# Performance work log

Measured on AMD Instinct MI355X. Metric: run time of the kernel, lower is better.

## Reference

```python
import jax, jax.numpy as jnp
import numpy as np

B, T, D_IN = 32, 32, 128
N_SLOTS, M_LEN = 512, 64
NUM_SHIFT, NUM_READ, NUM_WRITE = 3, 4, 1
CTRL_DIM = 256
READ_HEAD_LEN = 3 + M_LEN + NUM_SHIFT            # k, beta, g, s, gamma
WRITE_HEAD_LEN = READ_HEAD_LEN + 2 * M_LEN       # + erase, add vectors
INSTR_DIM = NUM_READ * READ_HEAD_LEN + NUM_WRITE * WRITE_HEAD_LEN


def setup_inputs() -> dict:
    key = jax.random.key(0)
    ks = jax.random.split(key, 4)
    def glorot(k, shape):
        lim = np.sqrt(6.0 / (shape[0] + shape[1])).astype(np.float32)
        return jax.random.uniform(k, shape, jnp.float32, -lim, lim)
    return {
        "x": jax.random.normal(ks[0], (B, T, D_IN), jnp.float32),
        "Wc": glorot(ks[1], (D_IN + NUM_READ * M_LEN, CTRL_DIM)),
        "bc": jnp.zeros((CTRL_DIM,), jnp.float32),
        "heads_kernel": glorot(ks[2], (CTRL_DIM, INSTR_DIM)),
        "heads_bias": jnp.zeros((INSTR_DIM,), jnp.float32),
    }


def _parse_heads(h):
    # h: (B, H, 3 + M + S) -> k, beta, g, s, gamma per _get_weight_vector
    k = h[..., :M_LEN]
    b = jnp.exp(h[..., M_LEN])
    g = jax.nn.sigmoid(h[..., M_LEN + 1])
    s = jax.nn.softmax(h[..., M_LEN + 2:M_LEN + 2 + NUM_SHIFT], axis=-1)
    t = jax.nn.softplus(h[..., M_LEN + 2 + NUM_SHIFT]) + 1.0
    return k, b, g, s, t


def _address(Mem, w_prev, k, b, g, s, t):
    # Mem:(B,N,M) k:(B,H,M) w_prev:(B,H,N) b,g,t:(B,H) s:(B,H,S)
    eps = 1e-8
    Mn = jnp.linalg.norm(Mem, axis=-1)                       # (B,N)
    kn = jnp.linalg.norm(k, axis=-1)                         # (B,H)
    sim = jnp.einsum('bhm,bnm->bhn', k, Mem) / (kn[..., None] * Mn[:, None, :] + eps)
    wc = jax.nn.softmax(b[..., None] * sim, axis=-1)         # content
    wg = g[..., None] * wc + (1.0 - g[..., None]) * w_prev   # gate
    half = NUM_SHIFT // 2                                    # circular shift conv
    wsh = sum(s[..., i:i + 1] * jnp.roll(wg, i - half, axis=-1) for i in range(NUM_SHIFT))
    wt = wsh ** t[..., None]                                 # sharpen
    return wt / (jnp.sum(wt, axis=-1, keepdims=True) + eps)


def _ntm_forward(x, Wc, bc, heads_kernel, heads_bias):
    def step(carry, x_t):
        r, rw, ww, Mem = carry
        # dense controller on [x_t, old read vectors]
        ctrl_in = jnp.concatenate([x_t, r.reshape(B, -1)], axis=-1)
        h = jnp.tanh(ctrl_in @ Wc + bc)                      # controller_out == instr
        instr = h @ heads_kernel + heads_bias                # (B, INSTR_DIM)
        rh = instr[:, :NUM_READ * READ_HEAD_LEN].reshape(B, NUM_READ, READ_HEAD_LEN)
        wh = instr[:, NUM_READ * READ_HEAD_LEN:].reshape(B, NUM_WRITE, WRITE_HEAD_LEN)
        rw_n = _address(Mem, rw, *_parse_heads(rh))
        ww_n = _address(Mem, ww, *_parse_heads(wh[..., :READ_HEAD_LEN]))
        e = wh[..., READ_HEAD_LEN:READ_HEAD_LEN + M_LEN]     # raw erase (no sigmoid, as in source)
        a = wh[..., READ_HEAD_LEN + M_LEN:]                  # raw add
        # erase all heads, then add all heads (source loops erase first)
        Mem = Mem * jnp.prod(1.0 - ww_n[..., :, None] * e[..., None, :], axis=1)
        Mem = Mem + jnp.einsum('bwn,bwm->bnm', ww_n, a)
        r_n = jnp.einsum('bnm,brn->brm', Mem, rw_n)          # read
        return (r_n, rw_n, ww_n, Mem), h

    init = (jnp.zeros((B, NUM_READ, M_LEN), jnp.float32),
            jnp.zeros((B, NUM_READ, N_SLOTS), jnp.float32),
            jnp.zeros((B, NUM_WRITE, N_SLOTS), jnp.float32),
            jnp.zeros((B, N_SLOTS, M_LEN), jnp.float32))
    _, outs = jax.lax.scan(step, init, jnp.swapaxes(x, 0, 1))  # time-major
    return outs[-1]  # return_sequences=False -> last controller output (B, CTRL_DIM)


def reference(x, Wc, bc, heads_kernel, heads_bias):
    return _ntm_forward(x, Wc, bc, heads_kernel, heads_bias)
```

## Files before the change

### kernel.cpp

```cpp
#include <hip/hip_runtime.h>
#include <math.h>

#define BB 32
#define TT 32
#define D_INX 128
#define NSLOT 512
#define MLEN 64
#define NREAD 4
#define NHEAD 5
#define CDIM 256
#define IDIM 478
#define NT 1024

#define HKB_OFF 196608


struct SMem {
    float mem[NSLOT * MLEN];
    float wread4[NSLOT * 4];
    float wwrite[NSLOT];
    float mn[NSLOT];
    float ctrl[512];
    float h[CDIM];
    float instr[480];
    float xpart[CDIM];
    float u[2560];
};

__device__ __forceinline__ unsigned short f2bf(float f) {
    unsigned u = __float_as_uint(f);
    return (unsigned short)((u + 0x7fffu + ((u >> 16) & 1u)) >> 16);
}

__device__ __forceinline__ int permcol(int c) {
    if (c < 280) { int h = c / 70, m = c - h * 70;
        return (m < 64) ? h * 64 + m : 448 + h * 6 + (m - 64); }
    if (c < 344) return 256 + (c - 280);
    if (c < 350) return 472 + (c - 344);
    if (c < 414) return 320 + (c - 350);
    return 384 + (c - 414);
}

__global__ void pack_kernel(const float* __restrict__ Wc, const float* __restrict__ Hk,
                            unsigned short* __restrict__ wctb, unsigned short* __restrict__ hkb)
{
    int idx = blockIdx.x * 256 + threadIdx.x;
    if (idx < 384 * 256) {
        int i = idx >> 8, col = idx & 255;
        wctb[((i >> 3) * 256 + col) * 8 + (i & 7)] = f2bf(Wc[idx]);
    }
    if (idx < 256 * 478) {
        int i = idx / 478, c = idx - i * 478;
        hkb[((i >> 3) * 478 + permcol(c)) * 8 + (i & 7)] = f2bf(Hk[idx]);
    }
}

#define BFU_DOT(wv, cA, cB, acc) do {                                           \
    unsigned _u0 = (wv).x, _u1 = (wv).y, _u2 = (wv).z, _u3 = (wv).w;            \
    acc += __uint_as_float(_u0 << 16) * (cA).x + __uint_as_float(_u0 & 0xffff0000u) * (cA).y; \
    acc += __uint_as_float(_u1 << 16) * (cA).z + __uint_as_float(_u1 & 0xffff0000u) * (cA).w; \
    acc += __uint_as_float(_u2 << 16) * (cB).x + __uint_as_float(_u2 & 0xffff0000u) * (cB).y; \
    acc += __uint_as_float(_u3 << 16) * (cB).z + __uint_as_float(_u3 & 0xffff0000u) * (cB).w; \
} while (0)

#define L2E 1.4426950408889634f
#define LN2 0.6931471805599453f

__global__ __launch_bounds__(NT, 4)
void ntm_kernel(const float* __restrict__ x,
                const float* __restrict__ bc,
                const float* __restrict__ hb,
                const unsigned short* __restrict__ wctb,
                const unsigned short* __restrict__ hkb,
                float* __restrict__ out)
{
    extern __shared__ float smem_f[];
    SMem* sc = (SMem*)smem_f;

    const int b    = blockIdx.x;
    const int tid  = threadIdx.x;
    const int lane = tid & 63;
    const int wave = tid >> 6;

    float hbv = 0.f;
    if (tid >= 256 && tid < 256 + IDIM) {
        int j = tid - 256, c;
        if (j < 320) { int h = j >> 6, m = j & 63; c = (h < 4) ? h * 70 + m : 280 + m; }
        else if (j < 384) c = 350 + (j - 320);
        else if (j < 448) c = 414 + (j - 384);
        else { int q = j - 448; int h = q / 6, i = q - h * 6;
               c = (h < 4) ? h * 70 + 64 + i : 344 + i; }
        hbv = hb[c];
    }
    float bcv1 = (tid < CDIM) ? bc[tid] : 0.f;
    float bcv4 = (tid >= 320 && tid < 576) ? bc[tid - 320] : 0.f;

    {
        float4 z4 = make_float4(0.f, 0.f, 0.f, 0.f);
        float4* m4 = (float4*)sc->mem;
        for (int i = tid; i < NSLOT * MLEN / 4; i += NT) m4[i] = z4;
        if (tid < NSLOT) {
            ((float4*)sc->wread4)[tid] = z4;
            sc->wwrite[tid] = 0.f;
            sc->mn[tid] = 0.f;
            sc->ctrl[tid] = (tid < D_INX) ? x[(size_t)b * TT * D_INX + tid] : 0.f;
        }
    }
    __syncthreads();
    if (tid < CDIM) {
        const uint4* wq = (const uint4*)wctb + tid;
        const float4* xa = (const float4*)sc->ctrl;
        float acc = bcv1;
#pragma unroll
        for (int cc = 0; cc < 16; ++cc) {
            uint4 wv = wq[cc * 256];
            BFU_DOT(wv, xa[2 * cc], xa[2 * cc + 1], acc);
        }
        sc->xpart[tid] = acc;
    }
    __syncthreads();

    for (int t = 0; t < TT; ++t) {
        {
            int col = tid & 255, kb = tid >> 8;
            const uint4* wq = (const uint4*)wctb + (16 + kb * 8) * 256 + col;
            const float4* ra = (const float4*)(sc->ctrl + 256) + kb * 16;
            float acc = 0.f;
#pragma unroll
            for (int cc = 0; cc < 8; ++cc) {
                uint4 wv = wq[cc * 256];
                BFU_DOT(wv, ra[2 * cc], ra[2 * cc + 1], acc);
            }
            sc->u[kb * 256 + col] = acc;
        }
        __syncthreads();

        if (tid < CDIM) {
            float acc = sc->xpart[tid] + sc->u[tid] + sc->u[256 + tid]
                      + sc->u[512 + tid] + sc->u[768 + tid];
            float av = fabsf(acc);
            float ex = __builtin_amdgcn_exp2f(av * (2.f * L2E));
            float r1 = 1.f - 2.f / (ex + 1.f);
            float hv = (acc < 0.f) ? -r1 : r1;
            sc->h[tid] = hv;
            if (t == TT - 1) out[(size_t)b * CDIM + tid] = hv;
        } else if (tid < 256 + IDIM) {
            sc->instr[tid - 256] = hbv;
        }
        if (t == TT - 1) break;
        __syncthreads();

        {
            int col = tid & 511, kb = tid >> 9;
            if (col < IDIM) {
                const uint4* wq = (const uint4*)hkb + kb * 16 * IDIM + col;
                const float4* h4 = (const float4*)sc->h + kb * 32;
                float acc = 0.f;
#pragma unroll
                for (int cc = 0; cc < 16; ++cc) {
                    uint4 wv = wq[cc * IDIM];
                    BFU_DOT(wv, h4[2 * cc], h4[2 * cc + 1], acc);
                }
                atomicAdd(&sc->instr[col], acc);
            } else if (tid >= 990 && tid < 1022) {
                int i = tid - 990;
                ((float4*)(sc->ctrl + (((t + 1) & 1) << 7)))[i] =
                    ((const float4*)(x + ((size_t)b * TT + t + 1) * D_INX))[i];
            }
        }
        __syncthreads();

        {
            int n = tid >> 1, half = tid & 1, nx = n & 15;
            const float4* m4 = (const float4*)sc->mem + n * 16;
            const float4* kb4 = (const float4*)sc->instr;
            float d0 = 0.f, d1 = 0.f, d2 = 0.f, d3 = 0.f, d4 = 0.f;
#pragma unroll
            for (int jj = 0; jj < 8; ++jj) {
                int j = half * 8 + jj;
                float4 mv = m4[j ^ nx];
                float4 k0 = kb4[j], k1 = kb4[16 + j], k2 = kb4[32 + j],
                       k3 = kb4[48 + j], kw = kb4[64 + j];
                d0 += mv.x * k0.x + mv.y * k0.y + mv.z * k0.z + mv.w * k0.w;
                d1 += mv.x * k1.x + mv.y * k1.y + mv.z * k1.z + mv.w * k1.w;
                d2 += mv.x * k2.x + mv.y * k2.y + mv.z * k2.z + mv.w * k2.w;
                d3 += mv.x * k3.x + mv.y * k3.y + mv.z * k3.z + mv.w * k3.w;
                d4 += mv.x * kw.x + mv.y * kw.y + mv.z * kw.z + mv.w * kw.w;
            }
            d0 += __shfl_xor(d0, 1); d1 += __shfl_xor(d1, 1); d2 += __shfl_xor(d2, 1);
            d3 += __shfl_xor(d3, 1); d4 += __shfl_xor(d4, 1);
            if (half == 0) {
                sc->u[n] = d0; sc->u[512 + n] = d1; sc->u[1024 + n] = d2;
                sc->u[1536 + n] = d3; sc->u[2048 + n] = d4;
            }
        }
        __syncthreads();

        if (wave < NHEAD) {
            const int h = wave;
            const float* sb = sc->instr + 448 + h * 6;
            float kv = sc->instr[h * 64 + lane];
            float sq = kv * kv;
#pragma unroll
            for (int off = 32; off; off >>= 1) sq += __shfl_xor(sq, off);
            float kn = sqrtf(sq);
            float beta = __expf(sb[0]);
            float g = 1.f / (1.f + __expf(-sb[1]));
            float v0 = sb[2], v1 = sb[3], v2 = sb[4];
            float mx3 = fmaxf(v0, fmaxf(v1, v2));
            float e0 = __expf(v0 - mx3), e1 = __expf(v1 - mx3), e2 = __expf(v2 - mx3);
            float inv3 = 1.f / (e0 + e1 + e2);
            float s0 = e0 * inv3, s1 = e1 * inv3, s2 = e2 * inv3;
            float tv = sb[5];
            float tp = fmaxf(tv, 0.f)
                     + LN2 * __builtin_amdgcn_logf(1.f + __builtin_amdgcn_exp2f(-fabsf(tv) * L2E))
                     + 1.f;

            float uu[8];
#pragma unroll
            for (int j = 0; j < 8; ++j) {
                int slot = j * 64 + lane;
                float d = sc->u[h * NSLOT + slot];
                uu[j] = beta * d / (kn * sc->mn[slot] + 1e-8f);
            }
            float m = uu[0];
#pragma unroll
            for (int j = 1; j < 8; ++j) m = fmaxf(m, uu[j]);
#pragma unroll
            for (int off = 32; off; off >>= 1) m = fmaxf(m, __shfl_xor(m, off));
            float ev[8]; float Z = 0.f;
#pragma unroll
            for (int j = 0; j < 8; ++j) { ev[j] = __expf(uu[j] - m); Z += ev[j]; }
#pragma unroll
            for (int off = 32; off; off >>= 1) Z += __shfl_xor(Z, off);
            float invZ = 1.f / Z;
            float wg[8];
#pragma unroll
            for (int j = 0; j < 8; ++j) {
                int n = j * 64 + lane;
                float wp = (h < 4) ? sc->wread4[n * 4 + h] : sc->wwrite[n];
                wg[j] = g * ev[j] * invZ + (1.f - g) * wp;
            }
            int lm = (lane + 63) & 63, lp = (lane + 1) & 63;
            float rm[8], rp[8], b63[8], b0[8];
#pragma unroll
            for (int j = 0; j < 8; ++j) {
                rm[j]  = __shfl(wg[j], lm);
                rp[j]  = __shfl(wg[j], lp);
                b63[j] = __shfl(wg[j], 63);
                b0[j]  = __shfl(wg[j], 0);
            }
            if (lane == 0) {
#pragma unroll
                for (int j = 0; j < 8; ++j) rm[j] = b63[(j + 7) & 7];
            }
            if (lane == 63) {
#pragma unroll
                for (int j = 0; j < 8; ++j) rp[j] = b0[(j + 1) & 7];
            }
            float wt[8]; float S = 0.f;
#pragma unroll
            for (int j = 0; j < 8; ++j) {
                float wsh = s0 * rp[j] + s1 * wg[j] + s2 * rm[j];
                wt[j] = __builtin_amdgcn_exp2f(tp * __builtin_amdgcn_logf(wsh));
                S += wt[j];
            }
#pragma unroll
            for (int off = 32; off; off >>= 1) S += __shfl_xor(S, off);
            float invS = 1.f / (S + 1e-8f);
            if (h < 4) {
#pragma unroll
                for (int j = 0; j < 8; ++j)
                    sc->wread4[(j * 64 + lane) * 4 + h] = wt[j] * invS;
            } else {
#pragma unroll
                for (int j = 0; j < 8; ++j)
                    sc->wwrite[j * 64 + lane] = wt[j] * invS;
            }
        } else if (wave < 9) {
            int col = tid - 320;
            const uint4* wq = (const uint4*)wctb + col;
            const float4* xa = (const float4*)(sc->ctrl + (((t + 1) & 1) << 7));
            float acc = bcv4;
#pragma unroll
            for (int cc = 0; cc < 16; ++cc) {
                uint4 wv = wq[cc * 256];
                BFU_DOT(wv, xa[2 * cc], xa[2 * cc + 1], acc);
            }
            sc->xpart[col] = acc;
        } else if (wave == 9) {
            ((float4*)(sc->ctrl + 256))[lane] = make_float4(0.f, 0.f, 0.f, 0.f);
        }
        __syncthreads();

        {
            int n = tid >> 1, half = tid & 1, nx = n & 15;
            float4* m4 = (float4*)sc->mem + n * 16;
            const float4* e4 = (const float4*)(sc->instr + 320);
            const float4* a4 = (const float4*)(sc->instr + 384);
            float wv = sc->wwrite[n];
            float nsq = 0.f;
#pragma unroll
            for (int jj = 0; jj < 8; ++jj) {
                int j = half * 8 + jj;
                float4 mv = m4[j ^ nx];
                float4 ev = e4[j], av = a4[j];
                mv.x = mv.x * (1.f - wv * ev.x) + wv * av.x;
                mv.y = mv.y * (1.f - wv * ev.y) + wv * av.y;
                mv.z = mv.z * (1.f - wv * ev.z) + wv * av.z;
                mv.w = mv.w * (1.f - wv * ev.w) + wv * av.w;
                nsq += mv.x * mv.x + mv.y * mv.y + mv.z * mv.z + mv.w * mv.w;
                m4[j ^ nx] = mv;
            }
            nsq += __shfl_xor(nsq, 1);
            if (half == 0) sc->mn[n] = sqrtf(nsq);
        }
        __syncthreads();

        {
            int rg = lane >> 4, j = lane & 15;
            int base = wave * 32;
            float4 ac0 = make_float4(0.f,0.f,0.f,0.f), ac1 = ac0, ac2 = ac0, ac3 = ac0;
#pragma unroll
            for (int i = 0; i < 8; ++i) {
                int n = base + 4 * i + rg;
                float4 mv = ((const float4*)sc->mem)[n * 16 + (j ^ (n & 15))];
                float4 wv = ((const float4*)sc->wread4)[n];
                ac0.x += wv.x * mv.x; ac0.y += wv.x * mv.y; ac0.z += wv.x * mv.z; ac0.w += wv.x * mv.w;
                ac1.x += wv.y * mv.x; ac1.y += wv.y * mv.y; ac1.z += wv.y * mv.z; ac1.w += wv.y * mv.w;
                ac2.x += wv.z * mv.x; ac2.y += wv.z * mv.y; ac2.z += wv.z * mv.z; ac2.w += wv.z * mv.w;
                ac3.x += wv.w * mv.x; ac3.y += wv.w * mv.y; ac3.z += wv.w * mv.z; ac3.w += wv.w * mv.w;
            }
            float af[16] = { ac0.x, ac0.y, ac0.z, ac0.w, ac1.x, ac1.y, ac1.z, ac1.w,
                             ac2.x, ac2.y, ac2.z, ac2.w, ac3.x, ac3.y, ac3.z, ac3.w };
#pragma unroll
            for (int q = 0; q < 16; ++q) {
                af[q] += __shfl_xor(af[q], 16);
                af[q] += __shfl_xor(af[q], 32);
            }
            float sx = (rg == 0) ? af[0] : (rg == 1) ? af[4] : (rg == 2) ? af[8]  : af[12];
            float sy = (rg == 0) ? af[1] : (rg == 1) ? af[5] : (rg == 2) ? af[9]  : af[13];
            float sz = (rg == 0) ? af[2] : (rg == 1) ? af[6] : (rg == 2) ? af[10] : af[14];
            float sw = (rg == 0) ? af[3] : (rg == 1) ? af[7] : (rg == 2) ? af[11] : af[15];
            float* rdst = sc->ctrl + 256 + rg * 64 + j * 4;
            atomicAdd(&rdst[0], sx);
            atomicAdd(&rdst[1], sy);
            atomicAdd(&rdst[2], sz);
            atomicAdd(&rdst[3], sw);
        }
        __syncthreads();
    }
}

extern "C" void kernel_launch(void* const* d_in, const int* in_sizes, int n_in,
                              void* d_out, int out_size, void* d_ws, size_t ws_size,
                              hipStream_t stream) {
    const float* x  = (const float*)d_in[0];
    const float* Wc = (const float*)d_in[1];
    const float* bc = (const float*)d_in[2];
    const float* Hk = (const float*)d_in[3];
    const float* hb = (const float*)d_in[4];
    float* out = (float*)d_out;

    unsigned short* wctb = (unsigned short*)d_ws;
    unsigned short* hkb  = (unsigned short*)((char*)d_ws + HKB_OFF);

    static_assert(sizeof(SMem) <= 163840, "LDS overflow");
    (void)hipFuncSetAttribute((const void*)ntm_kernel,
                              hipFuncAttributeMaxDynamicSharedMemorySize,
                              (int)sizeof(SMem));

    hipLaunchKernelGGL(pack_kernel, dim3(478), dim3(256), 0, stream, Wc, Hk, wctb, hkb);
    hipLaunchKernelGGL(ntm_kernel, dim3(BB), dim3(NT), sizeof(SMem), stream,
                       x, bc, hb, wctb, hkb, out);
}
```

Measured before the change: 923.3 us.

## Reduce controller matvecs with wave shuffles instead of shared partials and atomics

Reworks the controller dense layer so each wave owns 16 output columns split across four k-slices and reduces them with cross-lane shuffles. This removes the shared-memory partial buffer and one block-wide barrier per timestep, and the tanh is applied inside the same phase. The heads matvec now maps 32 columns per wave with two k-halves combined by a shuffle, replacing shared-memory atomicAdd, and the bias is added directly. The launch-bounds occupancy hint is also dropped, which may change register allocation.

```diff
diff --git a/kernel.cpp b/kernel.cpp
--- a/kernel.cpp
+++ b/kernel.cpp
@@ -66,7 +66,7 @@
 #define L2E 1.4426950408889634f
 #define LN2 0.6931471805599453f
 
-__global__ __launch_bounds__(NT, 4)
+__global__ __launch_bounds__(NT)
 void ntm_kernel(const float* __restrict__ x,
                 const float* __restrict__ bc,
                 const float* __restrict__ hb,
@@ -82,9 +82,15 @@
     const int lane = tid & 63;
     const int wave = tid >> 6;
 
+    const int col1 = (wave << 4) | (lane & 15);
+    const int ks   = lane >> 4;
+    const int col2 = (wave << 5) | (lane & 31);
+    const int sl   = lane >> 5;
+
+    const float bcv1 = bc[col1];
     float hbv = 0.f;
-    if (tid >= 256 && tid < 256 + IDIM) {
-        int j = tid - 256, c;
+    if (wave < 15 && sl == 0 && col2 < IDIM) {
+        int j = col2, c;
         if (j < 320) { int h = j >> 6, m = j & 63; c = (h < 4) ? h * 70 + m : 280 + m; }
         else if (j < 384) c = 350 + (j - 320);
         else if (j < 448) c = 414 + (j - 384);
@@ -92,8 +98,7 @@
                c = (h < 4) ? h * 70 + 64 + i : 344 + i; }
         hbv = hb[c];
     }
-    float bcv1 = (tid < CDIM) ? bc[tid] : 0.f;
-    float bcv4 = (tid >= 320 && tid < 576) ? bc[tid - 320] : 0.f;
+    const float bcv4 = (tid >= 320 && tid < 576) ? bc[tid - 320] : 0.f;
 
     {
         float4 z4 = make_float4(0.f, 0.f, 0.f, 0.f);
@@ -110,7 +115,7 @@
     if (tid < CDIM) {
         const uint4* wq = (const uint4*)wctb + tid;
         const float4* xa = (const float4*)sc->ctrl;
-        float acc = bcv1;
+        float acc = bc[tid];
 #pragma unroll
         for (int cc = 0; cc < 16; ++cc) {
             uint4 wv = wq[cc * 256];
@@ -122,51 +127,46 @@
 
     for (int t = 0; t < TT; ++t) {
         {
-            int col = tid & 255, kb = tid >> 8;
-            const uint4* wq = (const uint4*)wctb + (16 + kb * 8) * 256 + col;
-            const float4* ra = (const float4*)(sc->ctrl + 256) + kb * 16;
+            const float4* rb = (const float4*)(sc->ctrl + 256);
             float acc = 0.f;
 #pragma unroll
             for (int cc = 0; cc < 8; ++cc) {
-                uint4 wv = wq[cc * 256];
-                BFU_DOT(wv, ra[2 * cc], ra[2 * cc + 1], acc);
-            }
-            sc->u[kb * 256 + col] = acc;
-        }
-        __syncthreads();
-
-        if (tid < CDIM) {
-            float acc = sc->xpart[tid] + sc->u[tid] + sc->u[256 + tid]
-                      + sc->u[512 + tid] + sc->u[768 + tid];
-            float av = fabsf(acc);
-            float ex = __builtin_amdgcn_exp2f(av * (2.f * L2E));
-            float r1 = 1.f - 2.f / (ex + 1.f);
-            float hv = (acc < 0.f) ? -r1 : r1;
-            sc->h[tid] = hv;
-            if (t == TT - 1) out[(size_t)b * CDIM + tid] = hv;
-        } else if (tid < 256 + IDIM) {
-            sc->instr[tid - 256] = hbv;
+                int ce = (cc + ks) & 7;
+                int ch = ks * 8 + ce;
+                uint4 wv = ((const uint4*)wctb)[(16 + ch) * 256 + col1];
+                BFU_DOT(wv, rb[2 * ch], rb[2 * ch + 1], acc);
+            }
+            acc += __shfl_xor(acc, 16);
+            acc += __shfl_xor(acc, 32);
+            if (lane < 16) {
+                acc += sc->xpart[col1];
+                float av = fabsf(acc);
+                float ex = __builtin_amdgcn_exp2f(av * (2.f * L2E));
+                float r1 = 1.f - 2.f / (ex + 1.f);
+                float hv = (acc < 0.f) ? -r1 : r1;
+                sc->h[col1] = hv;
+                if (t == TT - 1) out[(size_t)b * CDIM + col1] = hv;
+            }
         }
         if (t == TT - 1) break;
         __syncthreads();
 
-        {
-            int col = tid & 511, kb = tid >> 9;
-            if (col < IDIM) {
-                const uint4* wq = (const uint4*)hkb + kb * 16 * IDIM + col;
-                const float4* h4 = (const float4*)sc->h + kb * 32;
+        if (wave < 15) {
+            if (col2 < IDIM) {
+                const uint4* wq = (const uint4*)hkb + sl * 16 * IDIM + col2;
+                const float4* h4 = (const float4*)sc->h + sl * 32;
                 float acc = 0.f;
 #pragma unroll
                 for (int cc = 0; cc < 16; ++cc) {
                     uint4 wv = wq[cc * IDIM];
                     BFU_DOT(wv, h4[2 * cc], h4[2 * cc + 1], acc);
                 }
-                atomicAdd(&sc->instr[col], acc);
-            } else if (tid >= 990 && tid < 1022) {
-                int i = tid - 990;
-                ((float4*)(sc->ctrl + (((t + 1) & 1) << 7)))[i] =
-                    ((const float4*)(x + ((size_t)b * TT + t + 1) * D_INX))[i];
-            }
+                acc += __shfl_xor(acc, 32);
+                if (sl == 0) sc->instr[col2] = acc + hbv;
+            }
+        } else if (lane < 32) {
+            ((float4*)(sc->ctrl + (((t + 1) & 1) << 7)))[lane] =
+                ((const float4*)(x + ((size_t)b * TT + t + 1) * D_INX))[lane];
         }
         __syncthreads();
 
```

Measured after the change: 918.7 us. Within noise of the previous version (-0.5%).
